# Performance work log

Hardware: AMD Instinct MI355X
Metric: run time of the kernel (lower is better)

Reference implementation:

```python
import jax, jax.numpy as jnp
import numpy as np

B, S, D, H = 2, 2048, 1024, 16
DH = D // H

def setup_inputs() -> dict:
    key = jax.random.key(0)
    ks = jax.random.split(key, 12)
    def lin(kw, kb, fan_in):
        bound = 1.0 / np.sqrt(fan_in)
        W = jax.random.uniform(kw, (D, D), jnp.float32, -bound, bound)
        b = jax.random.uniform(kb, (D,), jnp.float32, -bound, bound)
        return W, b
    Wq, bq = lin(ks[0], ks[1], D)
    Wk, bk = lin(ks[2], ks[3], D)
    Wv, bv = lin(ks[4], ks[5], D)
    Wo, bo = lin(ks[6], ks[7], D)
    q = jax.random.normal(ks[8], (B, S, D), jnp.float32)
    k = jax.random.normal(ks[9], (B, S, D), jnp.float32)
    v = jax.random.normal(ks[10], (B, S, D), jnp.float32)
    # causal mask (1 = keep, 0 = masked), broadcastable to [B,H,S,S]
    mask = jnp.tril(jnp.ones((S, S), jnp.int32))[None, None, :, :]
    return {"q": q, "k": k, "v": v, "mask": mask,
            "Wq": Wq, "bq": bq, "Wk": Wk, "bk": bk,
            "Wv": Wv, "bv": bv, "Wo": Wo, "bo": bo}

def reference(q, k, v, mask, Wq, bq, Wk, bk, Wv, bv, Wo, bo):
    # projections: torch Linear is x @ W.T + b
    def split(x):  # [B,S,D] -> [B,H,S,DH]
        return x.reshape(B, S, H, DH).transpose(0, 2, 1, 3)
    qh = split(q @ Wq.T + bq)
    kh = split(k @ Wk.T + bk)
    vh = split(v @ Wv.T + bv)
    score = jnp.einsum('bhqd,bhkd->bhqk', qh, kh) / jnp.sqrt(jnp.float32(DH))
    score = jnp.where(mask == 0, jnp.float32(-1e9), score)
    attn = jax.nn.softmax(score, axis=-1)
    out = jnp.einsum('bhqk,bhkd->bhqd', attn, vh)
    out = out.transpose(0, 2, 1, 3).reshape(B, S, D)
    return out @ Wo.T + bo, attn
```

## Files before the change

### kernel.cpp

```cpp
#include <hip/hip_runtime.h>

#define S_LEN 2048
#define D_MODEL 1024
#define N_HEADS 16
#define D_HEAD 64
#define BATCH 2

typedef __bf16 bf16;
typedef __bf16 bf16x8 __attribute__((ext_vector_type(8)));
typedef __bf16 bf16x4 __attribute__((ext_vector_type(4)));
typedef float f32x4 __attribute__((ext_vector_type(4)));

__device__ __forceinline__ f32x4 mfma16(bf16x8 a, bf16x8 b, f32x4 c) {
  return __builtin_amdgcn_mfma_f32_16x16x32_bf16(a, b, c, 0, 0, 0);
}

__device__ __forceinline__ void gload16(const bf16* g, bf16* lds) {
  __builtin_amdgcn_global_load_lds((const __attribute__((address_space(1))) void*)g,
                                   (__attribute__((address_space(3))) void*)lds, 16, 0, 0);
}

__global__ __launch_bounds__(256) void cvt_all(
    const float* __restrict__ s0, const float* __restrict__ s1,
    const float* __restrict__ s2, const float* __restrict__ s3,
    const float* __restrict__ s4, const float* __restrict__ s5,
    const float* __restrict__ s6,
    bf16* __restrict__ d0, bf16* __restrict__ d1, bf16* __restrict__ d2,
    bf16* __restrict__ d3, bf16* __restrict__ d4, bf16* __restrict__ d5,
    bf16* __restrict__ d6) {
  const int y = blockIdx.y;
  const float* s;
  bf16* d;
  int n8;
  const int nQKV8 = BATCH * S_LEN * D_MODEL / 8;
  const int nW8 = D_MODEL * D_MODEL / 8;
  switch (y) {
    case 0: s = s0; d = d0; n8 = nQKV8; break;
    case 1: s = s1; d = d1; n8 = nQKV8; break;
    case 2: s = s2; d = d2; n8 = nQKV8; break;
    case 3: s = s3; d = d3; n8 = nW8; break;
    case 4: s = s4; d = d4; n8 = nW8; break;
    case 5: s = s5; d = d5; n8 = nW8; break;
    default: s = s6; d = d6; n8 = nW8; break;
  }
  const int i = blockIdx.x * blockDim.x + threadIdx.x;
  if (i >= n8) return;
  const f32x4 a = *(const f32x4*)(s + (size_t)i * 8);
  const f32x4 b = *(const f32x4*)(s + (size_t)i * 8 + 4);
  bf16x8 o;
  o[0] = (bf16)a[0]; o[1] = (bf16)a[1]; o[2] = (bf16)a[2]; o[3] = (bf16)a[3];
  o[4] = (bf16)b[0]; o[5] = (bf16)b[1]; o[6] = (bf16)b[2]; o[7] = (bf16)b[3];
  *(bf16x8*)(d + (size_t)i * 8) = o;
}

__device__ __forceinline__ void gemm_loop(const bf16* __restrict__ gA,
                                          const bf16* __restrict__ gB,
                                          bf16* As, bf16* Bs,
                                          f32x4 (&acc)[4][4], int tid) {
  const int l = tid & 63;
  const int w = tid >> 6;
  const int wr = w >> 1, wc = w & 1;
  const int lr = l & 15, lg = l >> 4;
  const int lrow8 = l >> 3;
  const int colg = ((l & 7) ^ (lrow8 & 7)) * 8;

  for (int k0 = 0; k0 < D_MODEL; k0 += 64) {
#pragma unroll
    for (int i = 0; i < 4; ++i) {
      const int c = w * 4 + i;
      const int row = c * 8 + lrow8;
      gload16(gA + (size_t)row * D_MODEL + k0 + colg, As + c * 512);
      gload16(gB + (size_t)row * D_MODEL + k0 + colg, Bs + c * 512);
    }
    __syncthreads();
#pragma unroll
    for (int half = 0; half < 2; ++half) {
      bf16x8 af[4], bfb[4];
#pragma unroll
      for (int mm = 0; mm < 4; ++mm) {
        const int row = wr * 64 + mm * 16 + lr;
        af[mm] = *(const bf16x8*)(As + row * 64 + ((half * 4 + lg) ^ (lr & 7)) * 8);
      }
#pragma unroll
      for (int nn = 0; nn < 4; ++nn) {
        const int row = wc * 64 + nn * 16 + lr;
        bfb[nn] = *(const bf16x8*)(Bs + row * 64 + ((half * 4 + lg) ^ (lr & 7)) * 8);
      }
#pragma unroll
      for (int mm = 0; mm < 4; ++mm)
#pragma unroll
        for (int nn = 0; nn < 4; ++nn)
          acc[mm][nn] = mfma16(af[mm], bfb[nn], acc[mm][nn]);
    }
    __syncthreads();
  }
}

__global__ __launch_bounds__(256) void gemm_qkv(
    const bf16* __restrict__ qb, const bf16* __restrict__ kb,
    const bf16* __restrict__ vb, const bf16* __restrict__ Wqb,
    const bf16* __restrict__ Wkb, const bf16* __restrict__ Wvb,
    const float* __restrict__ biasq, const float* __restrict__ biask,
    const float* __restrict__ biasv, bf16* __restrict__ qhw,
    bf16* __restrict__ khw, bf16* __restrict__ vtw) {
  __shared__ bf16 As[128 * 64];
  __shared__ bf16 Bs[128 * 64];
  __shared__ bf16 T[128][72];
  const int z = blockIdx.z;
  const bf16* A = (z == 0) ? qb : (z == 1) ? kb : vb;
  const bf16* W = (z == 0) ? Wqb : (z == 1) ? Wkb : Wvb;
  const float* bias = (z == 0) ? biasq : (z == 1) ? biask : biasv;
  const float scale = (z == 0) ? 0.125f : 1.0f;
  bf16* out = (z == 0) ? qhw : (z == 1) ? khw : vtw;

  const int tid = threadIdx.x;
  const int l = tid & 63;
  const int w = tid >> 6;
  const int wr = w >> 1, wc = w & 1;
  const int lr = l & 15, lg = l >> 4;

  f32x4 acc[4][4] = {};
  gemm_loop(A + ((size_t)blockIdx.x * 128) * D_MODEL,
            W + ((size_t)blockIdx.y * 128) * D_MODEL, As, Bs, acc, tid);

  const int b = (blockIdx.x * 128) >> 11;
  const int s0 = (blockIdx.x * 128) & 2047;

  if (z == 2) {
#pragma unroll
    for (int half = 0; half < 2; ++half) {
      if (wc == half) {
#pragma unroll
        for (int nn = 0; nn < 4; ++nn) {
          const int n = blockIdx.y * 128 + half * 64 + nn * 16 + lr;
          const float bv = bias[n];
#pragma unroll
          for (int mm = 0; mm < 4; ++mm)
#pragma unroll
            for (int r = 0; r < 4; ++r) {
              const int ml = wr * 64 + mm * 16 + lg * 4 + r;
              T[ml][nn * 16 + lr] = (bf16)(acc[mm][nn][r] + bv);
            }
        }
      }
      __syncthreads();
      const int d = tid & 63;
      const int sblk = (tid >> 6) * 32;
      const int hglob = blockIdx.y * 2 + half;
      bf16* orow = vtw + (((size_t)(b * N_HEADS + hglob)) * D_HEAD + d) * S_LEN + s0 + sblk;
#pragma unroll
      for (int j = 0; j < 4; ++j) {
        bf16x8 pk;
#pragma unroll
        for (int e = 0; e < 8; ++e) pk[e] = T[sblk + j * 8 + e][d];
        *(bf16x8*)(orow + j * 8) = pk;
      }
      __syncthreads();
    }
  } else {
#pragma unroll
    for (int half = 0; half < 2; ++half) {
      if (wc == half) {
#pragma unroll
        for (int nn = 0; nn < 4; ++nn) {
          const int n = blockIdx.y * 128 + half * 64 + nn * 16 + lr;
          const float bv = bias[n];
#pragma unroll
          for (int mm = 0; mm < 4; ++mm)
#pragma unroll
            for (int r = 0; r < 4; ++r) {
              const int ml = wr * 64 + mm * 16 + lg * 4 + r;
              T[ml][nn * 16 + lr] = (bf16)((acc[mm][nn][r] + bv) * scale);
            }
        }
      }
      __syncthreads();
      const int hglob = blockIdx.y * 2 + half;
      bf16* obase = out + ((size_t)(b * N_HEADS + hglob) * S_LEN + s0) * D_HEAD;
      const int rsub = tid >> 3;
      const int d8 = (tid & 7) * 8;
#pragma unroll
      for (int j = 0; j < 4; ++j) {
        const int row_l = j * 32 + rsub;
        *(bf16x8*)(obase + (size_t)row_l * D_HEAD + d8) = *(const bf16x8*)(&T[row_l][d8]);
      }
      __syncthreads();
    }
  }
}

__global__ __launch_bounds__(256) void gemm_out(const bf16* __restrict__ A,
                                                const bf16* __restrict__ W,
                                                const float* __restrict__ bias,
                                                float* __restrict__ out) {
  __shared__ bf16 As[128 * 64];
  __shared__ bf16 Bs[128 * 64];
  const int tid = threadIdx.x;
  const int l = tid & 63;
  const int w = tid >> 6;
  const int wr = w >> 1, wc = w & 1;
  const int lr = l & 15, lg = l >> 4;

  f32x4 acc[4][4] = {};
  gemm_loop(A + ((size_t)blockIdx.x * 128) * D_MODEL,
            W + ((size_t)blockIdx.y * 128) * D_MODEL, As, Bs, acc, tid);

  const int rowg0 = blockIdx.x * 128 + wr * 64;
  const int colg0 = blockIdx.y * 128 + wc * 64;
#pragma unroll
  for (int nn = 0; nn < 4; ++nn) {
    const int n = colg0 + nn * 16 + lr;
    const float bv = bias[n];
#pragma unroll
    for (int mm = 0; mm < 4; ++mm)
#pragma unroll
      for (int r = 0; r < 4; ++r) {
        const int m = rowg0 + mm * 16 + lg * 4 + r;
        out[(size_t)m * D_MODEL + n] = acc[mm][nn][r] + bv;
      }
  }
}

__device__ __forceinline__ void stage_strip(const bf16* __restrict__ src,
                                            size_t rstride, bf16* lds, int tid) {
#pragma unroll
  for (int rnd = 0; rnd < 2; ++rnd) {
    const int chunk = rnd * 256 + tid;
    const int row = chunk >> 3;
    const int c8 = chunk & 7;
    const int src8 = c8 ^ (row & 7);
    gload16(src + (size_t)row * rstride + src8 * 8, lds + chunk * 8);
  }
}

__global__ __launch_bounds__(256) void attn_flash(const bf16* __restrict__ qh,
                                                  const bf16* __restrict__ kh,
                                                  const bf16* __restrict__ vt,
                                                  bf16* __restrict__ ctx,
                                                  float* __restrict__ lbuf) {
  __shared__ bf16 Kb[2][64 * 64];
  __shared__ bf16 Vb[2][64 * 64];
  __shared__ bf16 P[4][16][72];
  const int tid = threadIdx.x;
  const int w = tid >> 6, l = tid & 63;
  const int lr = l & 15, lg = l >> 4;
  const int bh = blockIdx.y;
  const int bxx = blockIdx.x;
  const int qgroup = (bxx & 1) ? (31 - (bxx >> 1)) : (bxx >> 1);
  const int q0 = qgroup * 64 + w * 16;
  const int qrow = q0 + lr;
  const bf16* qp = qh + (size_t)bh * S_LEN * D_HEAD;
  const bf16* kp = kh + (size_t)bh * S_LEN * D_HEAD;
  const bf16* vp = vt + (size_t)bh * D_HEAD * S_LEN;

  const bf16x8 qf0 = *(const bf16x8*)(qp + (size_t)qrow * D_HEAD + lg * 8);
  const bf16x8 qf1 = *(const bf16x8*)(qp + (size_t)qrow * D_HEAD + 32 + lg * 8);

  const float NINF = -__builtin_inff();
  const int nfull = qgroup;
  const int x0 = (lg ^ (lr & 7)) * 8;
  const int x1 = ((4 | lg) ^ (lr & 7)) * 8;

  stage_strip(kp, D_HEAD, Kb[0], tid);
  stage_strip(vp, S_LEN, Vb[0], tid);
  __syncthreads();

  float lsum = 0.f;
  f32x4 oacc[4] = {};
  int cur = 0;

  for (int st = 0; st < nfull; ++st) {
    stage_strip(kp + (size_t)(st + 1) * 64 * D_HEAD, D_HEAD, Kb[cur ^ 1], tid);
    stage_strip(vp + (st + 1) * 64, S_LEN, Vb[cur ^ 1], tid);

    float ps = 0.f;
#pragma unroll
    for (int t = 0; t < 4; ++t) {
      const bf16* krow = Kb[cur] + (t * 16 + lr) * 64;
      f32x4 zz = {};
      zz = mfma16(*(const bf16x8*)(krow + x0), qf0, zz);
      zz = mfma16(*(const bf16x8*)(krow + x1), qf1, zz);
      bf16x4 pk;
#pragma unroll
      for (int r = 0; r < 4; ++r) {
        const float e = __expf(fminf(zz[r], 60.f));
        ps += e;
        pk[r] = (bf16)e;
      }
      *(bf16x4*)(&P[w][lr][t * 16 + lg * 4]) = pk;
    }
    ps += __shfl_xor(ps, 16);
    ps += __shfl_xor(ps, 32);
    lsum += ps;
    const bf16x8 pb0 = *(const bf16x8*)(&P[w][lr][lg * 8]);
    const bf16x8 pb1 = *(const bf16x8*)(&P[w][lr][32 + lg * 8]);
#pragma unroll
    for (int dt = 0; dt < 4; ++dt) {
      const bf16* vrow = Vb[cur] + (dt * 16 + lr) * 64;
      oacc[dt] = mfma16(*(const bf16x8*)(vrow + x0), pb0, oacc[dt]);
      oacc[dt] = mfma16(*(const bf16x8*)(vrow + x1), pb1, oacc[dt]);
    }
    __syncthreads();
    cur ^= 1;
  }

  {
    float ps = 0.f;
#pragma unroll
    for (int t = 0; t < 4; ++t) {
      bf16x4 pk;
      if (t <= w) {
        const bf16* krow = Kb[cur] + (t * 16 + lr) * 64;
        f32x4 zz = {};
        zz = mfma16(*(const bf16x8*)(krow + x0), qf0, zz);
        zz = mfma16(*(const bf16x8*)(krow + x1), qf1, zz);
#pragma unroll
        for (int r = 0; r < 4; ++r) {
          const float sv = (t == w && (lg * 4 + r) > lr) ? NINF : zz[r];
          const float e = __expf(fminf(sv, 60.f));
          ps += e;
          pk[r] = (bf16)e;
        }
      } else {
#pragma unroll
        for (int r = 0; r < 4; ++r) pk[r] = (bf16)0.f;
      }
      *(bf16x4*)(&P[w][lr][t * 16 + lg * 4]) = pk;
    }
    ps += __shfl_xor(ps, 16);
    ps += __shfl_xor(ps, 32);
    lsum += ps;
    const bf16x8 pb0 = *(const bf16x8*)(&P[w][lr][lg * 8]);
    const bf16x8 pb1 = *(const bf16x8*)(&P[w][lr][32 + lg * 8]);
#pragma unroll
    for (int dt = 0; dt < 4; ++dt) {
      const bf16* vrow = Vb[cur] + (dt * 16 + lr) * 64;
      oacc[dt] = mfma16(*(const bf16x8*)(vrow + x0), pb0, oacc[dt]);
      oacc[dt] = mfma16(*(const bf16x8*)(vrow + x1), pb1, oacc[dt]);
    }
  }

  const float invl = 1.0f / lsum;
  const int b = bh >> 4, h = bh & 15;
  bf16* crow = ctx + ((size_t)(b * S_LEN + qrow)) * D_MODEL + h * D_HEAD;
#pragma unroll
  for (int dt = 0; dt < 4; ++dt) {
    bf16x4 ov;
#pragma unroll
    for (int r = 0; r < 4; ++r) ov[r] = (bf16)(oacc[dt][r] * invl);
    *(bf16x4*)(crow + dt * 16 + lg * 4) = ov;
  }
  if (lg == 0) lbuf[(size_t)bh * S_LEN + qrow] = invl;
}

__global__ __launch_bounds__(256) void attn_mat(const bf16* __restrict__ qh,
                                                const bf16* __restrict__ kh,
                                                const float* __restrict__ lbuf,
                                                float* __restrict__ attn) {
  __shared__ bf16 Pt[64][264];
  const int tid = threadIdx.x;
  const int w = tid >> 6, l = tid & 63;
  const int lr = l & 15, lg = l >> 4;
  const int bh = blockIdx.z;
  const int q0 = blockIdx.x * 64;
  const int k0b = blockIdx.y * 256;
  float* ap = attn + (size_t)bh * S_LEN * S_LEN;

  if (k0b > q0 + 63) {
    const f32x4 zv = {};
#pragma unroll
    for (int j = 0; j < 4; ++j) {
      const int q = q0 + w * 16 + j * 4 + lg;
      float* rp = ap + (size_t)q * S_LEN + k0b + lr * 4;
#pragma unroll
      for (int sub = 0; sub < 4; ++sub)
        __builtin_nontemporal_store(zv, (f32x4*)(rp + sub * 64));
    }
    return;
  }

  const int k0 = k0b + w * 64;
  if (k0 <= q0 + 63) {
    const bf16* qp = qh + (size_t)bh * S_LEN * D_HEAD;
    const bf16* kp = kh + (size_t)bh * S_LEN * D_HEAD;
    float iv[4];
#pragma unroll
    for (int qs = 0; qs < 4; ++qs)
      iv[qs] = lbuf[(size_t)bh * S_LEN + q0 + qs * 16 + lr];
    bf16x8 kf[4][2], qf[4][2];
#pragma unroll
    for (int kt = 0; kt < 4; ++kt) {
      kf[kt][0] = *(const bf16x8*)(kp + (size_t)(k0 + kt * 16 + lr) * D_HEAD + lg * 8);
      kf[kt][1] = *(const bf16x8*)(kp + (size_t)(k0 + kt * 16 + lr) * D_HEAD + 32 + lg * 8);
    }
#pragma unroll
    for (int qs = 0; qs < 4; ++qs) {
      qf[qs][0] = *(const bf16x8*)(qp + (size_t)(q0 + qs * 16 + lr) * D_HEAD + lg * 8);
      qf[qs][1] = *(const bf16x8*)(qp + (size_t)(q0 + qs * 16 + lr) * D_HEAD + 32 + lg * 8);
    }
    f32x4 acc[4][4] = {};
#pragma unroll
    for (int qs = 0; qs < 4; ++qs)
#pragma unroll
      for (int kt = 0; kt < 4; ++kt) {
        acc[qs][kt] = mfma16(kf[kt][0], qf[qs][0], acc[qs][kt]);
        acc[qs][kt] = mfma16(kf[kt][1], qf[qs][1], acc[qs][kt]);
      }
#pragma unroll
    for (int qs = 0; qs < 4; ++qs) {
      const int q = q0 + qs * 16 + lr;
#pragma unroll
      for (int kt = 0; kt < 4; ++kt) {
        const int kbase = k0 + kt * 16 + lg * 4;
        bf16x4 pk;
#pragma unroll
        for (int r = 0; r < 4; ++r) {
          const float pv = (kbase + r > q)
                               ? 0.f
                               : __expf(fminf(acc[qs][kt][r], 60.f)) * iv[qs];
          pk[r] = (bf16)pv;
        }
        *(bf16x4*)(&Pt[qs * 16 + lr][w * 64 + kt * 16 + lg * 4]) = pk;
      }
    }
  } else {
    const bf16x4 z4 = {};
#pragma unroll
    for (int j = 0; j < 16; ++j)
      *(bf16x4*)(&Pt[j * 4 + lg][w * 64 + lr * 4]) = z4;
  }
  __syncthreads();

#pragma unroll
  for (int j = 0; j < 4; ++j) {
    const int rowl = w * 16 + j * 4 + lg;
    float* rp = ap + (size_t)(q0 + rowl) * S_LEN + k0b + lr * 4;
#pragma unroll
    for (int sub = 0; sub < 4; ++sub) {
      const bf16x4 pk = *(const bf16x4*)(&Pt[rowl][sub * 64 + lr * 4]);
      f32x4 o;
      o[0] = (float)pk[0]; o[1] = (float)pk[1];
      o[2] = (float)pk[2]; o[3] = (float)pk[3];
      __builtin_nontemporal_store(o, (f32x4*)(rp + sub * 64));
    }
  }
}

extern "C" void kernel_launch(void* const* d_in, const int* in_sizes, int n_in,
                              void* d_out, int out_size, void* d_ws, size_t ws_size,
                              hipStream_t stream) {
  (void)in_sizes; (void)n_in; (void)out_size; (void)ws_size;
  const float* q  = (const float*)d_in[0];
  const float* k  = (const float*)d_in[1];
  const float* v  = (const float*)d_in[2];
  const float* Wq = (const float*)d_in[4];
  const float* bq = (const float*)d_in[5];
  const float* Wk = (const float*)d_in[6];
  const float* bk = (const float*)d_in[7];
  const float* Wv = (const float*)d_in[8];
  const float* bv = (const float*)d_in[9];
  const float* Wo = (const float*)d_in[10];
  const float* bo = (const float*)d_in[11];

  float* outp = (float*)d_out;
  float* attn = outp + (size_t)BATCH * S_LEN * D_MODEL;

  char* ws = (char*)d_ws;
  bf16* qb   = (bf16*)(ws);
  bf16* kb   = (bf16*)(ws + (8u << 20));
  bf16* vb   = (bf16*)(ws + (16u << 20));
  bf16* qhw  = (bf16*)(ws + (24u << 20));
  bf16* Wqb  = (bf16*)(ws + (32u << 20));
  bf16* Wkb  = (bf16*)(ws + (34u << 20));
  bf16* Wvb  = (bf16*)(ws + (36u << 20));
  bf16* Wob  = (bf16*)(ws + (38u << 20));
  float* lbuf = (float*)(ws + (40u << 20));
  bf16* khw  = qb;
  bf16* vtw  = kb;
  bf16* ctxb = vb;

  dim3 bb(256);
  cvt_all<<<dim3(2048, 7), bb, 0, stream>>>(q, k, v, Wq, Wk, Wv, Wo,
                                            qb, kb, vb, Wqb, Wkb, Wvb, Wob);
  gemm_qkv<<<dim3(32, 8, 3), bb, 0, stream>>>(qb, kb, vb, Wqb, Wkb, Wvb,
                                              bq, bk, bv, qhw, khw, vtw);
  attn_flash<<<dim3(32, 32), bb, 0, stream>>>(qhw, khw, vtw, ctxb, lbuf);
  attn_mat<<<dim3(32, 8, 32), bb, 0, stream>>>(qhw, khw, lbuf, attn);
  gemm_out<<<dim3(32, 8), bb, 0, stream>>>(ctxb, Wob, bo, outp);
}
```

Measured before the change: 278.3 us.

## Fuse activation fp32->bf16 conversion into QKV GEMM and merge out-proj with attn-matrix kernel

The separate conversion pass for q/k/v activations is removed. The QKV GEMM now loads fp32 A tiles directly, converts them in registers and writes them to swizzled LDS, so only the weights still get a separate conversion kernel. The output projection GEMM and the attention-probability materialization kernel are merged into one launch, with the first 256 blocks doing the GEMM and the rest writing the attention matrix, so the two can overlap on the GPU. s_setprio hints are added around the MFMA sections in flash attention. In exchange, the A tile loads become synchronous register loads instead of async LDS loads, and GEMM A traffic is now fp32, which is read once per N tile.

```diff
diff --git a/kernel.cpp b/kernel.cpp
--- a/kernel.cpp
+++ b/kernel.cpp
@@ -20,31 +20,15 @@
                                    (__attribute__((address_space(3))) void*)lds, 16, 0, 0);
 }
 
-__global__ __launch_bounds__(256) void cvt_all(
+__global__ __launch_bounds__(256) void cvt_w(
     const float* __restrict__ s0, const float* __restrict__ s1,
     const float* __restrict__ s2, const float* __restrict__ s3,
-    const float* __restrict__ s4, const float* __restrict__ s5,
-    const float* __restrict__ s6,
     bf16* __restrict__ d0, bf16* __restrict__ d1, bf16* __restrict__ d2,
-    bf16* __restrict__ d3, bf16* __restrict__ d4, bf16* __restrict__ d5,
-    bf16* __restrict__ d6) {
+    bf16* __restrict__ d3) {
   const int y = blockIdx.y;
-  const float* s;
-  bf16* d;
-  int n8;
-  const int nQKV8 = BATCH * S_LEN * D_MODEL / 8;
-  const int nW8 = D_MODEL * D_MODEL / 8;
-  switch (y) {
-    case 0: s = s0; d = d0; n8 = nQKV8; break;
-    case 1: s = s1; d = d1; n8 = nQKV8; break;
-    case 2: s = s2; d = d2; n8 = nQKV8; break;
-    case 3: s = s3; d = d3; n8 = nW8; break;
-    case 4: s = s4; d = d4; n8 = nW8; break;
-    case 5: s = s5; d = d5; n8 = nW8; break;
-    default: s = s6; d = d6; n8 = nW8; break;
-  }
+  const float* s = (y == 0) ? s0 : (y == 1) ? s1 : (y == 2) ? s2 : s3;
+  bf16* d = (y == 0) ? d0 : (y == 1) ? d1 : (y == 2) ? d2 : d3;
   const int i = blockIdx.x * blockDim.x + threadIdx.x;
-  if (i >= n8) return;
   const f32x4 a = *(const f32x4*)(s + (size_t)i * 8);
   const f32x4 b = *(const f32x4*)(s + (size_t)i * 8 + 4);
   bf16x8 o;
@@ -96,9 +80,70 @@
   }
 }
 
+__device__ __forceinline__ void gemm_loop_af32(const float* __restrict__ gA32,
+                                               const bf16* __restrict__ gB,
+                                               bf16* As, bf16* Bs,
+                                               f32x4 (&acc)[4][4], int tid) {
+  const int l = tid & 63;
+  const int w = tid >> 6;
+  const int wr = w >> 1, wc = w & 1;
+  const int lr = l & 15, lg = l >> 4;
+  const int lrow8 = l >> 3;
+  const int colg = ((l & 7) ^ (lrow8 & 7)) * 8;
+
+  const int arow = tid >> 1;
+  const int ahalf = tid & 1;
+  const float* aptr = gA32 + (size_t)arow * D_MODEL + ahalf * 32;
+  bf16* awr = As + arow * 64;
+
+  for (int k0 = 0; k0 < D_MODEL; k0 += 64) {
+    f32x4 av[8];
+#pragma unroll
+    for (int c = 0; c < 8; ++c) av[c] = *(const f32x4*)(aptr + k0 + c * 4);
+#pragma unroll
+    for (int i = 0; i < 4; ++i) {
+      const int c = w * 4 + i;
+      const int row = c * 8 + lrow8;
+      gload16(gB + (size_t)row * D_MODEL + k0 + colg, Bs + c * 512);
+    }
+#pragma unroll
+    for (int c8 = 0; c8 < 4; ++c8) {
+      bf16x8 o;
+#pragma unroll
+      for (int e = 0; e < 4; ++e) {
+        o[e] = (bf16)av[c8 * 2][e];
+        o[e + 4] = (bf16)av[c8 * 2 + 1][e];
+      }
+      const int col16 = ahalf * 4 + c8;
+      *(bf16x8*)(awr + (col16 ^ (arow & 7)) * 8) = o;
+    }
+    __syncthreads();
+#pragma unroll
+    for (int half = 0; half < 2; ++half) {
+      bf16x8 af[4], bfb[4];
+#pragma unroll
+      for (int mm = 0; mm < 4; ++mm) {
+        const int row = wr * 64 + mm * 16 + lr;
+        af[mm] = *(const bf16x8*)(As + row * 64 + ((half * 4 + lg) ^ (lr & 7)) * 8);
+      }
+#pragma unroll
+      for (int nn = 0; nn < 4; ++nn) {
+        const int row = wc * 64 + nn * 16 + lr;
+        bfb[nn] = *(const bf16x8*)(Bs + row * 64 + ((half * 4 + lg) ^ (lr & 7)) * 8);
+      }
+#pragma unroll
+      for (int mm = 0; mm < 4; ++mm)
+#pragma unroll
+        for (int nn = 0; nn < 4; ++nn)
+          acc[mm][nn] = mfma16(af[mm], bfb[nn], acc[mm][nn]);
+    }
+    __syncthreads();
+  }
+}
+
 __global__ __launch_bounds__(256) void gemm_qkv(
-    const bf16* __restrict__ qb, const bf16* __restrict__ kb,
-    const bf16* __restrict__ vb, const bf16* __restrict__ Wqb,
+    const float* __restrict__ qf, const float* __restrict__ kf,
+    const float* __restrict__ vf, const bf16* __restrict__ Wqb,
     const bf16* __restrict__ Wkb, const bf16* __restrict__ Wvb,
     const float* __restrict__ biasq, const float* __restrict__ biask,
     const float* __restrict__ biasv, bf16* __restrict__ qhw,
@@ -107,7 +152,7 @@
   __shared__ bf16 Bs[128 * 64];
   __shared__ bf16 T[128][72];
   const int z = blockIdx.z;
-  const bf16* A = (z == 0) ? qb : (z == 1) ? kb : vb;
+  const float* A = (z == 0) ? qf : (z == 1) ? kf : vf;
   const bf16* W = (z == 0) ? Wqb : (z == 1) ? Wkb : Wvb;
   const float* bias = (z == 0) ? biasq : (z == 1) ? biask : biasv;
   const float scale = (z == 0) ? 0.125f : 1.0f;
@@ -120,8 +165,8 @@
   const int lr = l & 15, lg = l >> 4;
 
   f32x4 acc[4][4] = {};
-  gemm_loop(A + ((size_t)blockIdx.x * 128) * D_MODEL,
-            W + ((size_t)blockIdx.y * 128) * D_MODEL, As, Bs, acc, tid);
+  gemm_loop_af32(A + ((size_t)blockIdx.x * 128) * D_MODEL,
+                 W + ((size_t)blockIdx.y * 128) * D_MODEL, As, Bs, acc, tid);
 
   const int b = (blockIdx.x * 128) >> 11;
   const int s0 = (blockIdx.x * 128) & 2047;
@@ -186,38 +231,6 @@
       }
       __syncthreads();
     }
-  }
-}
-
-__global__ __launch_bounds__(256) void gemm_out(const bf16* __restrict__ A,
-                                                const bf16* __restrict__ W,
-                                                const float* __restrict__ bias,
-                                                float* __restrict__ out) {
-  __shared__ bf16 As[128 * 64];
-  __shared__ bf16 Bs[128 * 64];
-  const int tid = threadIdx.x;
-  const int l = tid & 63;
-  const int w = tid >> 6;
-  const int wr = w >> 1, wc = w & 1;
-  const int lr = l & 15, lg = l >> 4;
-
-  f32x4 acc[4][4] = {};
-  gemm_loop(A + ((size_t)blockIdx.x * 128) * D_MODEL,
-            W + ((size_t)blockIdx.y * 128) * D_MODEL, As, Bs, acc, tid);
-
-  const int rowg0 = blockIdx.x * 128 + wr * 64;
-  const int colg0 = blockIdx.y * 128 + wc * 64;
-#pragma unroll
-  for (int nn = 0; nn < 4; ++nn) {
-    const int n = colg0 + nn * 16 + lr;
-    const float bv = bias[n];
-#pragma unroll
-    for (int mm = 0; mm < 4; ++mm)
-#pragma unroll
-      for (int r = 0; r < 4; ++r) {
-        const int m = rowg0 + mm * 16 + lg * 4 + r;
-        out[(size_t)m * D_MODEL + n] = acc[mm][nn][r] + bv;
-      }
   }
 }
 
@@ -274,16 +287,23 @@
     stage_strip(vp + (st + 1) * 64, S_LEN, Vb[cur ^ 1], tid);
 
     float ps = 0.f;
+    __builtin_amdgcn_s_setprio(1);
+    f32x4 zz4[4];
 #pragma unroll
     for (int t = 0; t < 4; ++t) {
       const bf16* krow = Kb[cur] + (t * 16 + lr) * 64;
       f32x4 zz = {};
       zz = mfma16(*(const bf16x8*)(krow + x0), qf0, zz);
       zz = mfma16(*(const bf16x8*)(krow + x1), qf1, zz);
+      zz4[t] = zz;
+    }
+    __builtin_amdgcn_s_setprio(0);
+#pragma unroll
+    for (int t = 0; t < 4; ++t) {
       bf16x4 pk;
 #pragma unroll
       for (int r = 0; r < 4; ++r) {
-        const float e = __expf(fminf(zz[r], 60.f));
+        const float e = __expf(fminf(zz4[t][r], 60.f));
         ps += e;
         pk[r] = (bf16)e;
       }
@@ -294,12 +314,14 @@
     lsum += ps;
     const bf16x8 pb0 = *(const bf16x8*)(&P[w][lr][lg * 8]);
     const bf16x8 pb1 = *(const bf16x8*)(&P[w][lr][32 + lg * 8]);
+    __builtin_amdgcn_s_setprio(1);
 #pragma unroll
     for (int dt = 0; dt < 4; ++dt) {
       const bf16* vrow = Vb[cur] + (dt * 16 + lr) * 64;
       oacc[dt] = mfma16(*(const bf16x8*)(vrow + x0), pb0, oacc[dt]);
       oacc[dt] = mfma16(*(const bf16x8*)(vrow + x1), pb1, oacc[dt]);
     }
+    __builtin_amdgcn_s_setprio(0);
     __syncthreads();
     cur ^= 1;
   }
@@ -353,17 +375,48 @@
   if (lg == 0) lbuf[(size_t)bh * S_LEN + qrow] = invl;
 }
 
-__global__ __launch_bounds__(256) void attn_mat(const bf16* __restrict__ qh,
-                                                const bf16* __restrict__ kh,
-                                                const float* __restrict__ lbuf,
-                                                float* __restrict__ attn) {
-  __shared__ bf16 Pt[64][264];
+__global__ __launch_bounds__(256) void mat_out(
+    const bf16* __restrict__ qh, const bf16* __restrict__ kh,
+    const float* __restrict__ lbuf, float* __restrict__ attn,
+    const bf16* __restrict__ ctxA, const bf16* __restrict__ Wo,
+    const float* __restrict__ bo, float* __restrict__ outp) {
+  __shared__ __align__(16) char smem[34048];
+  const int bid = blockIdx.x;
   const int tid = threadIdx.x;
   const int w = tid >> 6, l = tid & 63;
   const int lr = l & 15, lg = l >> 4;
-  const int bh = blockIdx.z;
-  const int q0 = blockIdx.x * 64;
-  const int k0b = blockIdx.y * 256;
+
+  if (bid < 256) {
+    bf16* As = (bf16*)smem;
+    bf16* Bs = (bf16*)(smem + 16384);
+    const int bx = bid & 31, by = bid >> 5;
+    const int wr = w >> 1, wc = w & 1;
+    f32x4 acc[4][4] = {};
+    gemm_loop(ctxA + ((size_t)bx * 128) * D_MODEL,
+              Wo + ((size_t)by * 128) * D_MODEL, As, Bs, acc, tid);
+    const int rowg0 = bx * 128 + wr * 64;
+    const int colg0 = by * 128 + wc * 64;
+#pragma unroll
+    for (int nn = 0; nn < 4; ++nn) {
+      const int n = colg0 + nn * 16 + lr;
+      const float bv = bo[n];
+#pragma unroll
+      for (int mm = 0; mm < 4; ++mm)
+#pragma unroll
+        for (int r = 0; r < 4; ++r) {
+          const int m = rowg0 + mm * 16 + lg * 4 + r;
+          __builtin_nontemporal_store(acc[mm][nn][r] + bv,
+                                      outp + (size_t)m * D_MODEL + n);
+        }
+    }
+    return;
+  }
+
+  bf16* Pt = (bf16*)smem;
+  const int mid = bid - 256;
+  const int q0 = (mid & 31) * 64;
+  const int k0b = ((mid >> 5) & 7) * 256;
+  const int bh = mid >> 8;
   float* ap = attn + (size_t)bh * S_LEN * S_LEN;
 
   if (k0b > q0 + 63) {
@@ -420,14 +473,14 @@
                                : __expf(fminf(acc[qs][kt][r], 60.f)) * iv[qs];
           pk[r] = (bf16)pv;
         }
-        *(bf16x4*)(&Pt[qs * 16 + lr][w * 64 + kt * 16 + lg * 4]) = pk;
+        *(bf16x4*)(Pt + (qs * 16 + lr) * 264 + w * 64 + kt * 16 + lg * 4) = pk;
       }
     }
   } else {
     const bf16x4 z4 = {};
 #pragma unroll
     for (int j = 0; j < 16; ++j)
-      *(bf16x4*)(&Pt[j * 4 + lg][w * 64 + lr * 4]) = z4;
+      *(bf16x4*)(Pt + (j * 4 + lg) * 264 + w * 64 + lr * 4) = z4;
   }
   __syncthreads();
 
@@ -437,7 +490,7 @@
     float* rp = ap + (size_t)(q0 + rowl) * S_LEN + k0b + lr * 4;
 #pragma unroll
     for (int sub = 0; sub < 4; ++sub) {
-      const bf16x4 pk = *(const bf16x4*)(&Pt[rowl][sub * 64 + lr * 4]);
+      const bf16x4 pk = *(const bf16x4*)(Pt + rowl * 264 + sub * 64 + lr * 4);
       f32x4 o;
       o[0] = (float)pk[0]; o[1] = (float)pk[1];
       o[2] = (float)pk[2]; o[3] = (float)pk[3];
@@ -466,25 +519,21 @@
   float* attn = outp + (size_t)BATCH * S_LEN * D_MODEL;
 
   char* ws = (char*)d_ws;
-  bf16* qb   = (bf16*)(ws);
-  bf16* kb   = (bf16*)(ws + (8u << 20));
-  bf16* vb   = (bf16*)(ws + (16u << 20));
-  bf16* qhw  = (bf16*)(ws + (24u << 20));
+  bf16* qhw  = (bf16*)(ws);
+  bf16* khw  = (bf16*)(ws + (8u << 20));
+  bf16* vtw  = (bf16*)(ws + (16u << 20));
+  bf16* ctxb = (bf16*)(ws + (24u << 20));
   bf16* Wqb  = (bf16*)(ws + (32u << 20));
   bf16* Wkb  = (bf16*)(ws + (34u << 20));
   bf16* Wvb  = (bf16*)(ws + (36u << 20));
   bf16* Wob  = (bf16*)(ws + (38u << 20));
   float* lbuf = (float*)(ws + (40u << 20));
-  bf16* khw  = qb;
-  bf16* vtw  = kb;
-  bf16* ctxb = vb;
 
   dim3 bb(256);
-  cvt_all<<<dim3(2048, 7), bb, 0, stream>>>(q, k, v, Wq, Wk, Wv, Wo,
-                                            qb, kb, vb, Wqb, Wkb, Wvb, Wob);
-  gemm_qkv<<<dim3(32, 8, 3), bb, 0, stream>>>(qb, kb, vb, Wqb, Wkb, Wvb,
+  cvt_w<<<dim3(512, 4), bb, 0, stream>>>(Wq, Wk, Wv, Wo, Wqb, Wkb, Wvb, Wob);
+  gemm_qkv<<<dim3(32, 8, 3), bb, 0, stream>>>(q, k, v, Wqb, Wkb, Wvb,
                                               bq, bk, bv, qhw, khw, vtw);
   attn_flash<<<dim3(32, 32), bb, 0, stream>>>(qhw, khw, vtw, ctxb, lbuf);
-  attn_mat<<<dim3(32, 8, 32), bb, 0, stream>>>(qhw, khw, lbuf, attn);
-  gemm_out<<<dim3(32, 8), bb, 0, stream>>>(ctxb, Wob, bo, outp);
-}
+  mat_out<<<dim3(8448), bb, 0, stream>>>(qhw, khw, lbuf, attn,
+                                         ctxb, Wob, bo, outp);
+}
```

Result: no change. 277.0 us (-0.5%).
